# Kernel optimization log

Measured on AMD Instinct MI355X. Metric: run time of the kernel, lower is better.

Reference implementation:

```python
import math
import jax, jax.numpy as jnp
import numpy as np

DIM = 192
HEADS = 6
WIN = (16, 16)
N = WIN[0] * WIN[1]
B_ = 256
NW = 64
CPB_HIDDEN = 512


def _relative_coords_table(window_size):
    Wh, Ww = window_size
    h = np.arange(-(Wh - 1), Wh, dtype=np.float32)
    w = np.arange(-(Ww - 1), Ww, dtype=np.float32)
    table = np.stack(np.meshgrid(h, w, indexing='ij'), axis=-1)[None]  # (1, 2Wh-1, 2Ww-1, 2)
    table[..., 0] /= (Wh - 1)
    table[..., 1] /= (Ww - 1)
    table *= 8.0
    table = np.sign(table) * np.log2(np.abs(table) + 1.0) / np.log2(8.0)
    return table.astype(np.float32)


def _relative_position_index(window_size):
    Wh, Ww = window_size
    coords = np.stack(np.meshgrid(np.arange(Wh), np.arange(Ww), indexing='ij'))  # (2, Wh, Ww)
    flat = coords.reshape(2, -1)
    rel = flat[:, :, None] - flat[:, None, :]  # (2, N, N)
    rel = rel.transpose(1, 2, 0).astype(np.int64)
    rel[..., 0] += Wh - 1
    rel[..., 1] += Ww - 1
    rel[..., 0] *= 2 * Ww - 1
    return rel.sum(-1)  # (N, N)


def setup_inputs() -> dict:
    key = jax.random.key(0)
    ks = jax.random.split(key, 9)
    s = 1.0 / math.sqrt(DIM)
    inp = {
        'x': jax.random.normal(ks[0], (B_, N, DIM), dtype=jnp.float32),
        'mask': jax.random.normal(ks[1], (NW, N, N), dtype=jnp.float32),
        'qkv_w': jax.random.normal(ks[2], (3 * DIM, DIM), dtype=jnp.float32) * s,
        'qkv_b': jnp.zeros((3 * DIM,), dtype=jnp.float32),
        'proj_w': jax.random.normal(ks[3], (DIM, DIM), dtype=jnp.float32) * s,
        'proj_b': jnp.zeros((DIM,), dtype=jnp.float32),
        'logit_scale': jnp.full((HEADS, 1, 1), math.log(10.0), dtype=jnp.float32),
        'cpb_w1': jax.random.normal(ks[4], (CPB_HIDDEN, 2), dtype=jnp.float32) * (1.0 / math.sqrt(2.0)),
        'cpb_b1': jnp.zeros((CPB_HIDDEN,), dtype=jnp.float32),
        'cpb_w2': jax.random.normal(ks[5], (HEADS, CPB_HIDDEN), dtype=jnp.float32) * (1.0 / math.sqrt(CPB_HIDDEN)),
        'coords_table': jnp.asarray(_relative_coords_table(WIN)),
        'rel_index': jnp.asarray(_relative_position_index(WIN)),
    }
    return inp


def reference(x, mask, qkv_w, qkv_b, proj_w, proj_b, logit_scale,
              cpb_w1, cpb_b1, cpb_w2, coords_table, rel_index):
    Bw, n, C = x.shape
    H = logit_scale.shape[0]
    Dh = C // H
    eps = 1e-12

    qkv = x @ qkv_w.T + qkv_b                             # (B_, N, 3C)
    qkv = qkv.reshape(Bw, n, 3, H, Dh).transpose(2, 0, 3, 1, 4)
    q, k, v = qkv[0], qkv[1], qkv[2]                      # (B_, H, N, Dh)

    qn = q / jnp.maximum(jnp.linalg.norm(q, axis=-1, keepdims=True), eps)
    kn = k / jnp.maximum(jnp.linalg.norm(k, axis=-1, keepdims=True), eps)
    attn = jnp.einsum('bhnd,bhmd->bhnm', qn, kn)

    scale = jnp.exp(jnp.minimum(logit_scale, math.log(1.0 / 0.01)))  # (H,1,1)
    attn = attn * scale[None]

    # CPB MLP bias: (1, 2Wh-1, 2Ww-1, 2) -> (-1, H), gather, sigmoid-scale
    hbt = jax.nn.relu(coords_table @ cpb_w1.T + cpb_b1) @ cpb_w2.T   # (1, 2Wh-1, 2Ww-1, H)
    bias_table = hbt.reshape(-1, H)
    bias = bias_table[rel_index.reshape(-1)].reshape(n, n, H).transpose(2, 0, 1)
    attn = attn + 16.0 * jax.nn.sigmoid(bias)[None]

    nW = mask.shape[0]
    attn = attn.reshape(Bw // nW, nW, H, n, n) + mask[None, :, None]
    attn = attn.reshape(Bw, H, n, n)

    attn = jax.nn.softmax(attn, axis=-1)
    out = jnp.einsum('bhnm,bhmd->bhnd', attn, v)
    out = out.transpose(0, 2, 1, 3).reshape(Bw, n, C)
    return out @ proj_w.T + proj_b
```

## Files before the change

kernel.cpp:

```cpp
#include <hip/hip_runtime.h>

using bf16 = __bf16;
typedef bf16 bf16x4 __attribute__((ext_vector_type(4)));
typedef bf16 bf16x8 __attribute__((ext_vector_type(8)));
typedef float f32x4 __attribute__((ext_vector_type(4)));

__device__ __forceinline__ int swz192(int row, int col) {
  return row * 192 + (col ^ ((row & 7) << 3));
}
__device__ __forceinline__ int qk_idx(int row, int col) {
  return (row >> 1) * 64 + (row & 1) * 32 + (col ^ (((row >> 1) & 3) << 3));
}
__device__ __forceinline__ int vt_idx(int d, int n) {
  return d * 256 + (((n + ((d >> 3) << 4)) & 255) ^ ((d & 7) << 3));
}
__device__ __forceinline__ int p_idx4(int wv, int r, int c) {
  return wv * 1024 + r * 64 + (c ^ ((r & 7) << 3));
}

#define LOG2E 1.44269504088896f
#define GLOAD_LDS(src, dst)                                                     \
  __builtin_amdgcn_global_load_lds(                                             \
      (const __attribute__((address_space(1))) void*)(src),                     \
      (__attribute__((address_space(3))) void*)(dst), 16, 0, 0)

template <bool OUT_F32, bool NORM_QK, int NT>
__global__ __launch_bounds__(256) void k_gemm(const bf16* __restrict__ A,
                                              const bf16* __restrict__ W,
                                              const float* __restrict__ bias,
                                              const float* __restrict__ lsc,
                                              void* __restrict__ Op, int Ntot) {
  __shared__ bf16 As[64 * 192];
  __shared__ bf16 Bs[64 * 192];
  const int bid = blockIdx.x;
  const int xcd = bid & 7;
  const int j = bid >> 3;
  const int m0 = (xcd + 8 * (j / NT)) * 64;
  const int n0 = (j % NT) * 64;
  const int t = threadIdx.x;

#pragma unroll
  for (int i = 0; i < 6; ++i) {
    const int f = t + i * 256;
    const int row = f / 24, c8 = f % 24;
    const int csw = (c8 ^ (row & 7)) * 8;
    GLOAD_LDS(&A[(m0 + row) * 192 + csw], &As[f * 8]);
    GLOAD_LDS(&W[(n0 + row) * 192 + csw], &Bs[f * 8]);
  }
  __syncthreads();

  const int w = t >> 6, lane = t & 63, lo = lane & 15, hi = lane >> 4;
  const int wm = (w >> 1) * 32, wn = (w & 1) * 32;
  f32x4 acc[2][2];
#pragma unroll
  for (int a = 0; a < 2; ++a)
#pragma unroll
    for (int c = 0; c < 2; ++c) acc[a][c] = f32x4{0.f, 0.f, 0.f, 0.f};

#pragma unroll
  for (int ks = 0; ks < 6; ++ks) {
    const int k0 = ks * 32 + hi * 8;
    bf16x8 af[2], bfr[2];
#pragma unroll
    for (int ri = 0; ri < 2; ++ri)
      af[ri] = *reinterpret_cast<const bf16x8*>(&As[swz192(wm + ri * 16 + lo, k0)]);
#pragma unroll
    for (int ci = 0; ci < 2; ++ci)
      bfr[ci] = *reinterpret_cast<const bf16x8*>(&Bs[swz192(wn + ci * 16 + lo, k0)]);
#pragma unroll
    for (int ri = 0; ri < 2; ++ri)
#pragma unroll
      for (int ci = 0; ci < 2; ++ci)
        acc[ri][ci] = __builtin_amdgcn_mfma_f32_16x16x32_bf16(af[ri], bfr[ci], acc[ri][ci], 0, 0, 0);
  }

  if (NORM_QK) {
    const int cb = n0 + wn;
    const bool donorm = (cb < 384);
    float smul = 1.f;
    if (cb < 192)
      smul = expf(fminf(lsc[cb >> 5], 4.605170185988091f)) * LOG2E;
    const int col0 = cb + lo;
    const float b0 = bias[col0], b1 = bias[col0 + 16];
    bf16* O = (bf16*)Op;
#pragma unroll
    for (int ri = 0; ri < 2; ++ri)
#pragma unroll
      for (int rr = 0; rr < 4; ++rr) {
        float v0 = acc[ri][0][rr] + b0;
        float v1 = acc[ri][1][rr] + b1;
        if (donorm) {
          float ss = v0 * v0 + v1 * v1;
          ss += __shfl_xor(ss, 1, 16);
          ss += __shfl_xor(ss, 2, 16);
          ss += __shfl_xor(ss, 4, 16);
          ss += __shfl_xor(ss, 8, 16);
          const float rn = smul / fmaxf(sqrtf(ss), 1e-12f);
          v0 *= rn;
          v1 *= rn;
        }
        const int row = m0 + wm + ri * 16 + hi * 4 + rr;
        O[row * Ntot + col0] = (bf16)v0;
        O[row * Ntot + col0 + 16] = (bf16)v1;
      }
  } else {
#pragma unroll
    for (int ri = 0; ri < 2; ++ri)
#pragma unroll
      for (int ci = 0; ci < 2; ++ci) {
        const int col = n0 + wn + ci * 16 + lo;
        const float bv = bias[col];
#pragma unroll
        for (int rr = 0; rr < 4; ++rr) {
          const int row = m0 + wm + ri * 16 + hi * 4 + rr;
          const float val = acc[ri][ci][rr] + bv;
          if (OUT_F32)
            __builtin_nontemporal_store(val, &((float*)Op)[row * Ntot + col]);
          else
            ((bf16*)Op)[row * Ntot + col] = (bf16)val;
        }
      }
  }
}

__global__ void k_cpb1(const float* __restrict__ ct, const float* __restrict__ w1,
                       const float* __restrict__ b1, const float* __restrict__ w2,
                       float* __restrict__ bt) {
  int idx = blockIdx.x * 256 + threadIdx.x;
  if (idx >= 961 * 6) return;
  int r = idx / 6, hh = idx % 6;
  float t0 = ct[r * 2], t1 = ct[r * 2 + 1];
  float acc = 0.f;
  for (int j = 0; j < 512; ++j) {
    float hv = fmaf(w1[j * 2], t0, fmaf(w1[j * 2 + 1], t1, b1[j]));
    hv = fmaxf(hv, 0.f);
    acc = fmaf(hv, w2[hh * 512 + j], acc);
  }
  bt[idx] = acc;
}

__global__ __launch_bounds__(256) void k_prep(
    const float* __restrict__ x, bf16* __restrict__ xb,
    const float* __restrict__ qkv_w, bf16* __restrict__ qkv_wb,
    const float* __restrict__ proj_w, bf16* __restrict__ proj_wb,
    const float* __restrict__ mask, bf16* __restrict__ maskT,
    const float* __restrict__ bt, const int* __restrict__ rel,
    float* __restrict__ biasfT) {
  __shared__ float tile[64][65];
  const int bid = blockIdx.x;
  if (bid < 6216) {
    const float* in;
    bf16* o;
    int vb;
    if (bid < 6144) { in = x; o = xb; vb = bid; }
    else if (bid < 6198) { in = qkv_w; o = qkv_wb; vb = bid - 6144; }
    else { in = proj_w; o = proj_wb; vb = bid - 6198; }
    const int i = (vb * 256 + threadIdx.x) * 8;
    const f32x4 a = *reinterpret_cast<const f32x4*>(&in[i]);
    const f32x4 b = *reinterpret_cast<const f32x4*>(&in[i + 4]);
    bf16x8 v;
    v[0] = (bf16)a[0]; v[1] = (bf16)a[1]; v[2] = (bf16)a[2]; v[3] = (bf16)a[3];
    v[4] = (bf16)b[0]; v[5] = (bf16)b[1]; v[6] = (bf16)b[2]; v[7] = (bf16)b[3];
    *reinterpret_cast<bf16x8*>(&o[i]) = v;
  } else if (bid < 7240) {
    const int rem = bid - 6216;
    const int mb = rem >> 4;
    const int it = (rem & 15) >> 2, jt = rem & 3;
    const int tx = threadIdx.x & 63, ty = threadIdx.x >> 6;
    const float* mp = mask + mb * 65536;
#pragma unroll
    for (int rr = 0; rr < 16; ++rr)
      tile[rr * 4 + ty][tx] = mp[(it * 64 + rr * 4 + ty) * 256 + jt * 64 + tx];
    __syncthreads();
    bf16* op = maskT + mb * 65536;
#pragma unroll
    for (int rr = 0; rr < 16; ++rr)
      op[(jt * 64 + rr * 4 + ty) * 256 + it * 64 + tx] = (bf16)(LOG2E * tile[tx][rr * 4 + ty]);
  } else {
    const int idx = (bid - 7240) * 256 + threadIdx.x;
    const int hh = idx >> 16;
    const int jj = (idx >> 8) & 255;
    const int i = idx & 255;
    const float v = bt[rel[i * 256 + jj] * 6 + hh];
    biasfT[idx] = LOG2E * 16.f / (1.f + expf(-v));
  }
}

__global__ __launch_bounds__(256) void k_attn(const bf16* __restrict__ qkv,
                                              const bf16* __restrict__ maskT,
                                              const float* __restrict__ biasfT,
                                              bf16* __restrict__ aout) {
  __shared__ bf16 ksh[256 * 32];
  __shared__ bf16 vts[32 * 256];
  __shared__ bf16 ps[4 * 16 * 64];

  const int bid = blockIdx.x;
  const int x = bid & 7, i = bid >> 3;
  const int mb = x * 8 + i / 24;
  const int rem = i % 24;
  const int b = (rem / 6) * 64 + mb;
  const int h = rem % 6;
  const int t = threadIdx.x;

  const int rsub = t >> 2;
  const int c4s = t & 3;
#pragma unroll
  for (int p = 0; p < 4; ++p) {
    const int row = p * 64 + rsub;
    const int base = (b * 256 + row) * 576 + h * 32 + c4s * 8;
    *reinterpret_cast<bf16x8*>(&ksh[qk_idx(row, c4s * 8)]) =
        *reinterpret_cast<const bf16x8*>(&qkv[base + 192]);
    bf16x8 v = *reinterpret_cast<const bf16x8*>(&qkv[base + 384]);
#pragma unroll
    for (int jj = 0; jj < 8; ++jj) vts[vt_idx(c4s * 8 + jj, row)] = v[jj];
  }
  __syncthreads();

  const int w = t >> 6, lane = t & 63, lo = lane & 15, hi = lane >> 4;
  const float* bT = biasfT + (h << 16);
  const bf16* mT = maskT + (mb << 16);
  const bf16* qbase = qkv + (b * 256) * 576 + h * 32;

  bf16x8 afn = *reinterpret_cast<const bf16x8*>(&qbase[(w * 16 + lo) * 576 + hi * 8]);

  f32x4 bvp[4];
  bf16x4 mvp[4];
  {
    const int rbase0 = w * 16 + hi * 4;
#pragma unroll
    for (int c = 0; c < 4; ++c) {
      const int col = c * 16 + lo;
      bvp[c] = *reinterpret_cast<const f32x4*>(&bT[col * 256 + rbase0]);
      mvp[c] = *reinterpret_cast<const bf16x4*>(&mT[col * 256 + rbase0]);
    }
  }

  for (int rgi = 0; rgi < 4; ++rgi) {
    const int rg = rgi * 4 + w;
    const int rbase = rg * 16 + hi * 4;
    const bf16x8 af = afn;
    if (rgi < 3)
      afn = *reinterpret_cast<const bf16x8*>(&qbase[((rg + 4) * 16 + lo) * 576 + hi * 8]);

    f32x4 po0 = {0.f, 0.f, 0.f, 0.f}, po1 = {0.f, 0.f, 0.f, 0.f};
    float sum[4] = {0.f, 0.f, 0.f, 0.f};

#pragma unroll
    for (int ph = 0; ph < 4; ++ph) {
      f32x4 bv[4];
      bf16x4 mv[4];
#pragma unroll
      for (int c = 0; c < 4; ++c) { bv[c] = bvp[c]; mv[c] = mvp[c]; }
      if (ph < 3) {
#pragma unroll
        for (int c = 0; c < 4; ++c) {
          const int col = (ph + 1) * 64 + c * 16 + lo;
          bvp[c] = *reinterpret_cast<const f32x4*>(&bT[col * 256 + rbase]);
          mvp[c] = *reinterpret_cast<const bf16x4*>(&mT[col * 256 + rbase]);
        }
      } else if (rgi < 3) {
#pragma unroll
        for (int c = 0; c < 4; ++c) {
          const int col = c * 16 + lo;
          bvp[c] = *reinterpret_cast<const f32x4*>(&bT[col * 256 + rbase + 64]);
          mvp[c] = *reinterpret_cast<const bf16x4*>(&mT[col * 256 + rbase + 64]);
        }
      }
      bf16x8 kf[4];
#pragma unroll
      for (int c4i = 0; c4i < 4; ++c4i) {
        const int ct = ph * 4 + c4i;
        kf[c4i] = *reinterpret_cast<const bf16x8*>(&ksh[qk_idx(ct * 16 + lo, hi * 8)]);
      }
      f32x4 a[4];
#pragma unroll
      for (int c4i = 0; c4i < 4; ++c4i) {
        f32x4 z = {0.f, 0.f, 0.f, 0.f};
        a[c4i] = __builtin_amdgcn_mfma_f32_16x16x32_bf16(af, kf[c4i], z, 0, 0, 0);
      }
#pragma unroll
      for (int c4i = 0; c4i < 4; ++c4i)
#pragma unroll
        for (int rr = 0; rr < 4; ++rr) {
          const float s = a[c4i][rr] + bv[c4i][rr] + (float)mv[c4i][rr];
          const float p = exp2f(s);
          sum[rr] += p;
          ps[p_idx4(w, hi * 4 + rr, c4i * 16 + lo)] = (bf16)p;
        }
#pragma unroll
      for (int kb = 0; kb < 2; ++kb) {
        const bf16x8 pa = *reinterpret_cast<const bf16x8*>(&ps[p_idx4(w, lo, kb * 32 + hi * 8)]);
        const bf16x8 b0 = *reinterpret_cast<const bf16x8*>(&vts[vt_idx(lo, ph * 64 + kb * 32 + hi * 8)]);
        const bf16x8 b1 = *reinterpret_cast<const bf16x8*>(&vts[vt_idx(16 + lo, ph * 64 + kb * 32 + hi * 8)]);
        po0 = __builtin_amdgcn_mfma_f32_16x16x32_bf16(pa, b0, po0, 0, 0, 0);
        po1 = __builtin_amdgcn_mfma_f32_16x16x32_bf16(pa, b1, po1, 0, 0, 0);
      }
    }
#pragma unroll
    for (int rr = 0; rr < 4; ++rr) {
      float s = sum[rr];
      s += __shfl_xor(s, 1, 16);
      s += __shfl_xor(s, 2, 16);
      s += __shfl_xor(s, 4, 16);
      s += __shfl_xor(s, 8, 16);
      sum[rr] = 1.f / s;
    }
#pragma unroll
    for (int rr = 0; rr < 4; ++rr) {
      const int ob = (b * 256 + rbase + rr) * 192 + h * 32;
      aout[ob + lo] = (bf16)(po0[rr] * sum[rr]);
      aout[ob + 16 + lo] = (bf16)(po1[rr] * sum[rr]);
    }
  }
}

extern "C" void kernel_launch(void* const* d_in, const int* in_sizes, int n_in,
                              void* d_out, int out_size, void* d_ws, size_t ws_size,
                              hipStream_t stream) {
  const float* x      = (const float*)d_in[0];
  const float* mask   = (const float*)d_in[1];
  const float* qkv_w  = (const float*)d_in[2];
  const float* qkv_b  = (const float*)d_in[3];
  const float* proj_w = (const float*)d_in[4];
  const float* proj_b = (const float*)d_in[5];
  const float* lsc    = (const float*)d_in[6];
  const float* cpb_w1 = (const float*)d_in[7];
  const float* cpb_b1 = (const float*)d_in[8];
  const float* cpb_w2 = (const float*)d_in[9];
  const float* ctab   = (const float*)d_in[10];
  const int*   relidx = (const int*)d_in[11];

  char* ws = (char*)d_ws;
  bf16*  qkvb   = (bf16*)(ws);
  bf16*  xb     = (bf16*)(ws + 75497472);
  bf16*  aoutb  = (bf16*)(ws + 75497472);
  float* biasfT = (float*)(ws + 100663296);
  bf16*  maskTb = (bf16*)(ws + 102236160);
  float* bt     = (float*)(ws + 110624768);
  bf16*  qkv_wb = (bf16*)(ws + 110647840);
  bf16*  proj_wb= (bf16*)(ws + 110869024);

  k_cpb1<<<23, 256, 0, stream>>>(ctab, cpb_w1, cpb_b1, cpb_w2, bt);
  k_prep<<<8776, 256, 0, stream>>>(x, xb, qkv_w, qkv_wb, proj_w, proj_wb,
                                   mask, maskTb, bt, relidx, biasfT);
  k_gemm<false, true, 9><<<9216, 256, 0, stream>>>(xb, qkv_wb, qkv_b, lsc, qkvb, 576);
  k_attn<<<1536, 256, 0, stream>>>(qkvb, maskTb, biasfT, aoutb);
  k_gemm<true, false, 3><<<3072, 256, 0, stream>>>(aoutb, proj_wb, proj_b, nullptr,
                                                   (float*)d_out, 192);
}
```

Before: 212.4 us.

## Reuse A tile across multiple N tiles in GEMMs; fold bias+mask into MFMA accumulator

The GEMM kernel now loads each 64-row A tile into shared memory once and loops over NG column tiles of W, reloading only the B tile each iteration. This reduces grid size and redundant A traffic for both the QKV and projection GEMMs. In exchange it serialises the B loads inside each block, with an extra barrier per group and less parallelism. In the attention kernel, the relative-position bias plus mask is precomputed and passed as the MFMA accumulator init, which removes per-element adds after the matmul.

```diff
diff --git a/kernel.cpp b/kernel.cpp
--- a/kernel.cpp
+++ b/kernel.cpp
@@ -24,7 +24,7 @@
       (const __attribute__((address_space(1))) void*)(src),                     \
       (__attribute__((address_space(3))) void*)(dst), 16, 0, 0)
 
-template <bool OUT_F32, bool NORM_QK, int NT>
+template <bool OUT_F32, bool NORM_QK, int NT, int NG>
 __global__ __launch_bounds__(256) void k_gemm(const bf16* __restrict__ A,
                                               const bf16* __restrict__ W,
                                               const float* __restrict__ bias,
@@ -34,10 +34,13 @@
   __shared__ bf16 Bs[64 * 192];
   const int bid = blockIdx.x;
   const int xcd = bid & 7;
-  const int j = bid >> 3;
-  const int m0 = (xcd + 8 * (j / NT)) * 64;
-  const int n0 = (j % NT) * 64;
+  const int jj = bid >> 3;
+  constexpr int NGRP = NT / NG;
+  const int m0 = (xcd + 8 * (jj / NGRP)) * 64;
+  const int nbase = (jj % NGRP) * NG;
   const int t = threadIdx.x;
+  const int w = t >> 6, lane = t & 63, lo = lane & 15, hi = lane >> 4;
+  const int wm = (w >> 1) * 32, wn = (w & 1) * 32;
 
 #pragma unroll
   for (int i = 0; i < 6; ++i) {
@@ -45,81 +48,90 @@
     const int row = f / 24, c8 = f % 24;
     const int csw = (c8 ^ (row & 7)) * 8;
     GLOAD_LDS(&A[(m0 + row) * 192 + csw], &As[f * 8]);
-    GLOAD_LDS(&W[(n0 + row) * 192 + csw], &Bs[f * 8]);
-  }
-  __syncthreads();
-
-  const int w = t >> 6, lane = t & 63, lo = lane & 15, hi = lane >> 4;
-  const int wm = (w >> 1) * 32, wn = (w & 1) * 32;
-  f32x4 acc[2][2];
-#pragma unroll
-  for (int a = 0; a < 2; ++a)
-#pragma unroll
-    for (int c = 0; c < 2; ++c) acc[a][c] = f32x4{0.f, 0.f, 0.f, 0.f};
-
-#pragma unroll
-  for (int ks = 0; ks < 6; ++ks) {
-    const int k0 = ks * 32 + hi * 8;
-    bf16x8 af[2], bfr[2];
-#pragma unroll
-    for (int ri = 0; ri < 2; ++ri)
-      af[ri] = *reinterpret_cast<const bf16x8*>(&As[swz192(wm + ri * 16 + lo, k0)]);
-#pragma unroll
-    for (int ci = 0; ci < 2; ++ci)
-      bfr[ci] = *reinterpret_cast<const bf16x8*>(&Bs[swz192(wn + ci * 16 + lo, k0)]);
-#pragma unroll
-    for (int ri = 0; ri < 2; ++ri)
+  }
+
+  for (int g = 0; g < NG; ++g) {
+    const int n0 = (nbase + g) * 64;
+    if (g > 0) __syncthreads();
+#pragma unroll
+    for (int i = 0; i < 6; ++i) {
+      const int f = t + i * 256;
+      const int row = f / 24, c8 = f % 24;
+      const int csw = (c8 ^ (row & 7)) * 8;
+      GLOAD_LDS(&W[(n0 + row) * 192 + csw], &Bs[f * 8]);
+    }
+    __syncthreads();
+
+    f32x4 acc[2][2];
+#pragma unroll
+    for (int a = 0; a < 2; ++a)
+#pragma unroll
+      for (int c = 0; c < 2; ++c) acc[a][c] = f32x4{0.f, 0.f, 0.f, 0.f};
+
+#pragma unroll
+    for (int ks = 0; ks < 6; ++ks) {
+      const int k0 = ks * 32 + hi * 8;
+      bf16x8 af[2], bfr[2];
+#pragma unroll
+      for (int ri = 0; ri < 2; ++ri)
+        af[ri] = *reinterpret_cast<const bf16x8*>(&As[swz192(wm + ri * 16 + lo, k0)]);
 #pragma unroll
       for (int ci = 0; ci < 2; ++ci)
-        acc[ri][ci] = __builtin_amdgcn_mfma_f32_16x16x32_bf16(af[ri], bfr[ci], acc[ri][ci], 0, 0, 0);
-  }
-
-  if (NORM_QK) {
-    const int cb = n0 + wn;
-    const bool donorm = (cb < 384);
-    float smul = 1.f;
-    if (cb < 192)
-      smul = expf(fminf(lsc[cb >> 5], 4.605170185988091f)) * LOG2E;
-    const int col0 = cb + lo;
-    const float b0 = bias[col0], b1 = bias[col0 + 16];
-    bf16* O = (bf16*)Op;
-#pragma unroll
-    for (int ri = 0; ri < 2; ++ri)
-#pragma unroll
-      for (int rr = 0; rr < 4; ++rr) {
-        float v0 = acc[ri][0][rr] + b0;
-        float v1 = acc[ri][1][rr] + b1;
-        if (donorm) {
-          float ss = v0 * v0 + v1 * v1;
-          ss += __shfl_xor(ss, 1, 16);
-          ss += __shfl_xor(ss, 2, 16);
-          ss += __shfl_xor(ss, 4, 16);
-          ss += __shfl_xor(ss, 8, 16);
-          const float rn = smul / fmaxf(sqrtf(ss), 1e-12f);
-          v0 *= rn;
-          v1 *= rn;
-        }
-        const int row = m0 + wm + ri * 16 + hi * 4 + rr;
-        O[row * Ntot + col0] = (bf16)v0;
-        O[row * Ntot + col0 + 16] = (bf16)v1;
-      }
-  } else {
-#pragma unroll
-    for (int ri = 0; ri < 2; ++ri)
-#pragma unroll
-      for (int ci = 0; ci < 2; ++ci) {
-        const int col = n0 + wn + ci * 16 + lo;
-        const float bv = bias[col];
+        bfr[ci] = *reinterpret_cast<const bf16x8*>(&Bs[swz192(wn + ci * 16 + lo, k0)]);
+#pragma unroll
+      for (int ri = 0; ri < 2; ++ri)
+#pragma unroll
+        for (int ci = 0; ci < 2; ++ci)
+          acc[ri][ci] = __builtin_amdgcn_mfma_f32_16x16x32_bf16(af[ri], bfr[ci], acc[ri][ci], 0, 0, 0);
+    }
+
+    if (NORM_QK) {
+      const int cb = n0 + wn;
+      const bool donorm = (cb < 384);
+      float smul = 1.f;
+      if (cb < 192)
+        smul = expf(fminf(lsc[cb >> 5], 4.605170185988091f)) * LOG2E;
+      const int col0 = cb + lo;
+      const float b0 = bias[col0], b1 = bias[col0 + 16];
+      bf16* O = (bf16*)Op;
+#pragma unroll
+      for (int ri = 0; ri < 2; ++ri)
 #pragma unroll
         for (int rr = 0; rr < 4; ++rr) {
+          float v0 = acc[ri][0][rr] + b0;
+          float v1 = acc[ri][1][rr] + b1;
+          if (donorm) {
+            float ss = v0 * v0 + v1 * v1;
+            ss += __shfl_xor(ss, 1, 16);
+            ss += __shfl_xor(ss, 2, 16);
+            ss += __shfl_xor(ss, 4, 16);
+            ss += __shfl_xor(ss, 8, 16);
+            const float rn = smul / fmaxf(sqrtf(ss), 1e-12f);
+            v0 *= rn;
+            v1 *= rn;
+          }
           const int row = m0 + wm + ri * 16 + hi * 4 + rr;
-          const float val = acc[ri][ci][rr] + bv;
-          if (OUT_F32)
-            __builtin_nontemporal_store(val, &((float*)Op)[row * Ntot + col]);
-          else
-            ((bf16*)Op)[row * Ntot + col] = (bf16)val;
-        }
-      }
+          O[row * Ntot + col0] = (bf16)v0;
+          O[row * Ntot + col0 + 16] = (bf16)v1;
+        }
+    } else {
+#pragma unroll
+      for (int ri = 0; ri < 2; ++ri)
+#pragma unroll
+        for (int ci = 0; ci < 2; ++ci) {
+          const int col = n0 + wn + ci * 16 + lo;
+          const float bv = bias[col];
+#pragma unroll
+          for (int rr = 0; rr < 4; ++rr) {
+            const int row = m0 + wm + ri * 16 + hi * 4 + rr;
+            const float val = acc[ri][ci][rr] + bv;
+            if (OUT_F32)
+              __builtin_nontemporal_store(val, &((float*)Op)[row * Ntot + col]);
+            else
+              ((bf16*)Op)[row * Ntot + col] = (bf16)val;
+          }
+        }
+    }
   }
 }
 
@@ -247,10 +259,14 @@
 
 #pragma unroll
     for (int ph = 0; ph < 4; ++ph) {
-      f32x4 bv[4];
-      bf16x4 mv[4];
-#pragma unroll
-      for (int c = 0; c < 4; ++c) { bv[c] = bvp[c]; mv[c] = mvp[c]; }
+      f32x4 cv[4];
+#pragma unroll
+      for (int c = 0; c < 4; ++c) {
+        cv[c][0] = bvp[c][0] + (float)mvp[c][0];
+        cv[c][1] = bvp[c][1] + (float)mvp[c][1];
+        cv[c][2] = bvp[c][2] + (float)mvp[c][2];
+        cv[c][3] = bvp[c][3] + (float)mvp[c][3];
+      }
       if (ph < 3) {
 #pragma unroll
         for (int c = 0; c < 4; ++c) {
@@ -274,16 +290,13 @@
       }
       f32x4 a[4];
 #pragma unroll
-      for (int c4i = 0; c4i < 4; ++c4i) {
-        f32x4 z = {0.f, 0.f, 0.f, 0.f};
-        a[c4i] = __builtin_amdgcn_mfma_f32_16x16x32_bf16(af, kf[c4i], z, 0, 0, 0);
-      }
-#pragma unroll
       for (int c4i = 0; c4i < 4; ++c4i)
+        a[c4i] = __builtin_amdgcn_mfma_f32_16x16x32_bf16(af, kf[c4i], cv[c4i], 0, 0, 0);
+#pragma unroll
+      for (int c4i = 0; c4i < 4; ++c4i)
 #pragma unroll
         for (int rr = 0; rr < 4; ++rr) {
-          const float s = a[c4i][rr] + bv[c4i][rr] + (float)mv[c4i][rr];
-          const float p = exp2f(s);
+          const float p = exp2f(a[c4i][rr]);
           sum[rr] += p;
           ps[p_idx4(w, hi * 4 + rr, c4i * 16 + lo)] = (bf16)p;
         }
@@ -343,8 +356,8 @@
   k_cpb1<<<23, 256, 0, stream>>>(ctab, cpb_w1, cpb_b1, cpb_w2, bt);
   k_prep<<<8776, 256, 0, stream>>>(x, xb, qkv_w, qkv_wb, proj_w, proj_wb,
                                    mask, maskTb, bt, relidx, biasfT);
-  k_gemm<false, true, 9><<<9216, 256, 0, stream>>>(xb, qkv_wb, qkv_b, lsc, qkvb, 576);
+  k_gemm<false, true, 9, 3><<<3072, 256, 0, stream>>>(xb, qkv_wb, qkv_b, lsc, qkvb, 576);
   k_attn<<<1536, 256, 0, stream>>>(qkvb, maskTb, biasfT, aoutb);
-  k_gemm<true, false, 3><<<3072, 256, 0, stream>>>(aoutb, proj_wb, proj_b, nullptr,
-                                                   (float*)d_out, 192);
-}
+  k_gemm<true, false, 3, 3><<<1024, 256, 0, stream>>>(aoutb, proj_wb, proj_b, nullptr,
+                                                      (float*)d_out, 192);
+}
```

New measurement: 232.9 us. +9.6%, slower.
